# Kernel optimization log

Measured on AMD Instinct MI355X. Metric: run time of the kernel, lower is better.

Reference implementation:

```python
import jax, jax.numpy as jnp
import numpy as np

N_USERS = 100_000
N_ITEMS = 50_000
CHANNEL = 64
N_EDGES = 2_000_000
LAYERS = 3


def setup_inputs() -> dict:
    key = jax.random.key(0)
    k1, k2, k3, k4, k5 = jax.random.split(key, 5)
    user_emb = jax.random.normal(k1, (N_USERS, CHANNEL), dtype=jnp.float32) * 0.1
    item_emb = jax.random.normal(k2, (N_ITEMS, CHANNEL), dtype=jnp.float32) * 0.1
    u_idx = jax.random.randint(k3, (N_EDGES,), 0, N_USERS, dtype=jnp.int32)
    i_idx = jax.random.randint(k4, (N_EDGES,), 0, N_ITEMS, dtype=jnp.int32)
    inter_edge = jnp.stack([u_idx, i_idx], axis=0)  # [2, E]
    inter_edge_w = jax.random.uniform(k5, (N_EDGES,), dtype=jnp.float32)
    return {
        "layers_num": LAYERS,
        "user_emb": user_emb,
        "item_emb": item_emb,
        "inter_edge": inter_edge,
        "inter_edge_w": inter_edge_w,
    }


def reference(layers_num, user_emb, item_emb, inter_edge, inter_edge_w):
    """AttnHGCN.forward_ui (eval mode: no sparse dropout).

    Per layer: gather neighbor embeddings via edge index, scale by edge weight,
    scatter-sum into the other side of the bipartite graph. Residual mean over
    all layer outputs (including input embeddings).
    """
    n_users = user_emb.shape[0]
    n_items = item_emb.shape[0]
    u_idx = inter_edge[0]  # [E] user index per edge
    i_idx = inter_edge[1]  # [E] item index per edge
    w = inter_edge_w[:, None]  # [E, 1]

    u, it = user_emb, item_emb
    user_acc, item_acc = user_emb, item_emb
    for _ in range(layers_num):
        item_agg = w * it[i_idx]  # [E, C] messages item -> user
        user_agg = w * u[u_idx]   # [E, C] messages user -> item
        u = jax.ops.segment_sum(item_agg, u_idx, num_segments=n_users)
        it = jax.ops.segment_sum(user_agg, i_idx, num_segments=n_items)
        user_acc = user_acc + u
        item_acc = item_acc + it

    inv = 1.0 / (layers_num + 1)
    return item_acc * inv, user_acc * inv
```

## Files before the change

kernel.cpp:

```cpp
#include <hip/hip_runtime.h>


constexpr int N_USERS = 100000;
constexpr int N_ITEMS = 50000;
constexpr int CH      = 64;
constexpr int N_EDGES = 2000000;
constexpr int LAYERS  = 3;
constexpr int NROWS   = N_USERS + N_ITEMS;
constexpr int NDIR    = 2 * N_EDGES;

constexpr int QEDGES  = N_EDGES / 4;
constexpr int NBLK    = (QEDGES + 1023) / 1024;

constexpr int FWIN    = 512;
constexpr int FROWS   = (NROWS + FWIN - 1) / FWIN;
constexpr int NFB     = FWIN * NBLK;

constexpr int WCAP    = 9216;

constexpr long long ITEM_ELEMS = (long long)N_ITEMS * CH;
constexpr long long USER_ELEMS = (long long)N_USERS * CH;
constexpr long long TOT_ELEMS  = ITEM_ELEMS + USER_ELEMS;

typedef int      v4i __attribute__((ext_vector_type(4)));
typedef float    v4f __attribute__((ext_vector_type(4)));
typedef float    v8f __attribute__((ext_vector_type(8)));
typedef _Float16 v4h __attribute__((ext_vector_type(4)));
typedef _Float16 v8h __attribute__((ext_vector_type(8)));

static __device__ __forceinline__ float w15_to_f(unsigned pk) {
  unsigned short us = (unsigned short)(pk & 0x7FFF);
  _Float16 h;
  __builtin_memcpy(&h, &us, 2);
  return (float)h;
}
static __device__ __forceinline__ unsigned pack_sw(int src, _Float16 hw) {
  unsigned short us;
  __builtin_memcpy(&us, &hw, 2);
  return ((unsigned)src << 15) | (us & 0x7FFF);
}


__global__ __launch_bounds__(256) void scanA_kernel(
    const int* __restrict__ in, int* __restrict__ out,
    int* __restrict__ blksums, int n) {
  __shared__ int sh[256];
  int t = threadIdx.x;
  int i = blockIdx.x * 256 + t;
  int v = (i < n) ? in[i] : 0;
  int x = v;
  sh[t] = x; __syncthreads();
  for (int d = 1; d < 256; d <<= 1) {
    int add = (t >= d) ? sh[t - d] : 0;
    __syncthreads();
    x += add; sh[t] = x;
    __syncthreads();
  }
  if (i < n) out[i] = x - v;
  if (t == 255) blksums[blockIdx.x] = x;
}

__global__ __launch_bounds__(1024) void scanB_kernel(int* __restrict__ blksums, int n2) {
  __shared__ int sh[1024];
  int t = threadIdx.x;
  int v = (t < n2) ? blksums[t] : 0;
  int x = v;
  sh[t] = x; __syncthreads();
  for (int d = 1; d < 1024; d <<= 1) {
    int add = (t >= d) ? sh[t - d] : 0;
    __syncthreads();
    x += add; sh[t] = x;
    __syncthreads();
  }
  if (t < n2) blksums[t] = x - v;
}

__global__ __launch_bounds__(256) void winscanC_kernel(
    int* __restrict__ out, const int* __restrict__ blksums, int n) {
  int i = blockIdx.x * 256 + threadIdx.x;
  if (i < n) out[i] += blksums[i >> 8];
}


__global__ __launch_bounds__(1024) void bincnt1024(
    const int* __restrict__ u_idx, const int* __restrict__ i_idx,
    int* __restrict__ blkfine) {
  __shared__ int cnt[FWIN];
  const int t = threadIdx.x;
  if (t < FWIN) cnt[t] = 0;
  __syncthreads();
  int q = blockIdx.x * 1024 + t;
  if (q < QEDGES) {
    v4i u  = *(const v4i*)(u_idx + 4 * (long long)q);
    v4i it = *(const v4i*)(i_idx + 4 * (long long)q);
    atomicAdd(&cnt[u.x / FROWS], 1);
    atomicAdd(&cnt[u.y / FROWS], 1);
    atomicAdd(&cnt[u.z / FROWS], 1);
    atomicAdd(&cnt[u.w / FROWS], 1);
    atomicAdd(&cnt[(N_USERS + it.x) / FROWS], 1);
    atomicAdd(&cnt[(N_USERS + it.y) / FROWS], 1);
    atomicAdd(&cnt[(N_USERS + it.z) / FROWS], 1);
    atomicAdd(&cnt[(N_USERS + it.w) / FROWS], 1);
  }
  __syncthreads();
  if (t < FWIN) blkfine[(long long)t * NBLK + blockIdx.x] = cnt[t];
}

__global__ __launch_bounds__(256) void fineoff_ext(
    const int* __restrict__ blkfine, int* __restrict__ fineoff) {
  int i = blockIdx.x * 256 + threadIdx.x;
  if (i < FWIN) fineoff[i] = blkfine[(long long)i * NBLK];
  if (i == FWIN) fineoff[FWIN] = NDIR;
}

__global__ __launch_bounds__(1024) void segwrite1024(
    const int* __restrict__ u_idx, const int* __restrict__ i_idx,
    const float* __restrict__ wv, const int* __restrict__ blkfine,
    int* __restrict__ segkey, _Float16* __restrict__ segw) {
  extern __shared__ char smem[];
  int*            skey = (int*)smem;
  _Float16*       sw   = (_Float16*)(skey + 8192);
  unsigned short* sfin = (unsigned short*)(sw + 8192);
  int*            cnt  = (int*)(sfin + 8192);

  const int t   = threadIdx.x;
  const int blk = blockIdx.x;
  if (t < FWIN) cnt[t] = 0;
  __syncthreads();

  int q = blk * 1024 + t;
  bool valid = (q < QEDGES);
  int key8[8], fin8[8], rank8[8];
  _Float16 hw8[8];
  if (valid) {
    v4i u  = *(const v4i*)(u_idx + 4 * (long long)q);
    v4i it = *(const v4i*)(i_idx + 4 * (long long)q);
    v4f w  = *(const v4f*)(wv + 4 * (long long)q);
    int rows[8], srcs[8];
    float ws[8];
    rows[0] = u.x; rows[1] = u.y; rows[2] = u.z; rows[3] = u.w;
    srcs[0] = it.x; srcs[1] = it.y; srcs[2] = it.z; srcs[3] = it.w;
    rows[4] = N_USERS + it.x; rows[5] = N_USERS + it.y;
    rows[6] = N_USERS + it.z; rows[7] = N_USERS + it.w;
    srcs[4] = u.x; srcs[5] = u.y; srcs[6] = u.z; srcs[7] = u.w;
    ws[0] = w.x; ws[1] = w.y; ws[2] = w.z; ws[3] = w.w;
    ws[4] = w.x; ws[5] = w.y; ws[6] = w.z; ws[7] = w.w;
#pragma unroll
    for (int k = 0; k < 8; ++k) {
      int fin = rows[k] / FROWS;
      int dl  = rows[k] - fin * FROWS;
      fin8[k]  = fin;
      key8[k]  = (dl << 18) | ((k >= 4) ? (1 << 17) : 0) | srcs[k];
      hw8[k]   = (_Float16)ws[k];
      rank8[k] = atomicAdd(&cnt[fin], 1);
    }
  }
  __syncthreads();

  int v = 0, x = 0;
  if (t < FWIN) { v = cnt[t]; x = v; }
  for (int d = 1; d < FWIN; d <<= 1) {
    int add = (t < FWIN && t >= d) ? cnt[t - d] : 0;
    __syncthreads();
    if (t < FWIN) { x += add; cnt[t] = x; }
    __syncthreads();
  }
  if (t < FWIN) cnt[t] = x - v;
  __syncthreads();

  if (valid) {
#pragma unroll
    for (int k = 0; k < 8; ++k) {
      int slot = cnt[fin8[k]] + rank8[k];
      skey[slot] = key8[k];
      sw[slot]   = hw8[k];
      sfin[slot] = (unsigned short)fin8[k];
    }
  }
  __syncthreads();

  const int ecount = 8 * min(1024, QEDGES - blk * 1024);
  for (int j = t; j < ecount; j += 1024) {
    int f = sfin[j];
    int gpos = blkfine[(long long)f * NBLK + blk] + (j - cnt[f]);
    segkey[gpos] = skey[j];
    segw[gpos]   = sw[j];
  }
}

__global__ __launch_bounds__(1024) void win_sort512(
    const int* __restrict__ segkey, const _Float16* __restrict__ segw,
    const int* __restrict__ fineoff, int* __restrict__ row_ptr,
    unsigned* __restrict__ csrp) {
  __shared__ unsigned        lkey[WCAP];
  __shared__ unsigned short  lwb[WCAP];
  __shared__ int             hist[FWIN];
  const int w   = blockIdx.x;
  const int wlo = w * FROWS;
  const int wsz = min(FROWS, NROWS - wlo);
  const int s0  = fineoff[w], s1 = fineoff[w + 1];
  const int n   = s1 - s0;
  const bool inlds = (n <= WCAP);
  const int t   = threadIdx.x;

  if (t < FWIN) hist[t] = 0;
  if (inlds) {
    for (int i = t; i < n; i += 1024) {
      lkey[i] = (unsigned)segkey[s0 + i];
      _Float16 h = segw[s0 + i];
      unsigned short us;
      __builtin_memcpy(&us, &h, 2);
      lwb[i] = us;
    }
  }
  __syncthreads();

  if (inlds) {
    for (int i = t; i < n; i += 1024) atomicAdd(&hist[lkey[i] >> 18], 1);
  } else {
    for (int i = t; i < n; i += 1024)
      atomicAdd(&hist[((unsigned)segkey[s0 + i]) >> 18], 1);
  }
  __syncthreads();

  int v = 0, x = 0;
  if (t < FWIN) { v = hist[t]; x = v; }
  for (int d = 1; d < FWIN; d <<= 1) {
    int add = (t < FWIN && t >= d) ? hist[t - d] : 0;
    __syncthreads();
    if (t < FWIN) { x += add; hist[t] = x; }
    __syncthreads();
  }
  __syncthreads();
  int base = x - v;
  if (t < wsz) row_ptr[wlo + t] = s0 + base;
  if (w == FWIN - 1 && t == 0) row_ptr[NROWS] = NDIR;
  if (t < FWIN) hist[t] = s0 + base;
  __syncthreads();

  if (inlds) {
    for (int i = t; i < n; i += 1024) {
      unsigned key = lkey[i];
      int p = atomicAdd(&hist[key >> 18], 1);
      csrp[p] = ((key & 0x1FFFFu) << 15) | (lwb[i] & 0x7FFF);
    }
  } else {
    for (int i = t; i < n; i += 1024) {
      unsigned key = (unsigned)segkey[s0 + i];
      int p = atomicAdd(&hist[key >> 18], 1);
      csrp[p] = pack_sw(key & 0x1FFFF, segw[s0 + i]);
    }
  }
}

__global__ __launch_bounds__(256) void cvt_tab(
    const float* __restrict__ it, const float* __restrict__ u,
    _Float16* __restrict__ t0) {
  long long i = (long long)blockIdx.x * 256 + threadIdx.x;
  if (i >= TOT_ELEMS / 4) return;
  long long e = i * 4;
  const float* src = (e < ITEM_ELEMS) ? (it + e) : (u + (e - ITEM_ELEMS));
  v4f f = *(const v4f*)src;
  v4h h = {(_Float16)f.x, (_Float16)f.y, (_Float16)f.z, (_Float16)f.w};
  *(v4h*)(t0 + e) = h;
}

template <int MODE>
__global__ __launch_bounds__(256) void gather_fused(
    const _Float16* __restrict__ tab,
    _Float16* __restrict__ dst,
    const _Float16* __restrict__ e0,
    const _Float16* __restrict__ e1,
    float* __restrict__ out,
    const unsigned* __restrict__ csrp,
    const int* __restrict__ row_ptr) {
  int row = blockIdx.x * 4 + (threadIdx.x >> 6);
  if (row >= NROWS) return;
  int lane = threadIdx.x & 63;
  int slot = lane >> 3;
  int c8   = (lane & 7) * 8;

  const _Float16* gtab;
  long long own;
  if (row < N_USERS) {
    gtab = tab;
    own  = ITEM_ELEMS + (long long)row * CH;
  } else {
    gtab = tab + ITEM_ELEMS;
    own  = (long long)(row - N_USERS) * CH;
  }

  int beg = row_ptr[row], end = row_ptr[row + 1];
  float acc[8];
#pragma unroll
  for (int k = 0; k < 8; ++k) acc[k] = 0.f;
  int j = beg + slot;
  for (; j + 8 < end; j += 16) {
    unsigned p0 = csrp[j];
    unsigned p1 = csrp[j + 8];
    v8h h0 = *(const v8h*)(gtab + (long long)(p0 >> 15) * CH + c8);
    v8h h1 = *(const v8h*)(gtab + (long long)(p1 >> 15) * CH + c8);
    float w0 = w15_to_f(p0);
    float w1 = w15_to_f(p1);
#pragma unroll
    for (int k = 0; k < 8; ++k) acc[k] += w0 * (float)h0[k];
#pragma unroll
    for (int k = 0; k < 8; ++k) acc[k] += w1 * (float)h1[k];
  }
  if (j < end) {
    unsigned p0 = csrp[j];
    float we = w15_to_f(p0);
    v8h h = *(const v8h*)(gtab + (long long)(p0 >> 15) * CH + c8);
#pragma unroll
    for (int k = 0; k < 8; ++k) acc[k] += we * (float)h[k];
  }
#pragma unroll
  for (int off = 8; off < 64; off <<= 1) {
#pragma unroll
    for (int k = 0; k < 8; ++k) acc[k] += __shfl_xor(acc[k], off, 64);
  }
  if (slot == 0) {
    if (MODE < 2) {
      v8h hd;
#pragma unroll
      for (int k = 0; k < 8; ++k) hd[k] = (_Float16)acc[k];
      *(v8h*)(dst + own + c8) = hd;
    } else {
      const float s = 1.0f / (LAYERS + 1);
      v8h a0 = *(const v8h*)(e0 + own + c8);
      v8h a1 = *(const v8h*)(e1 + own + c8);
      v8h a2 = *(const v8h*)(tab + own + c8);
      v8f o;
#pragma unroll
      for (int k = 0; k < 8; ++k)
        o[k] = ((float)a0[k] + (float)a1[k] + (float)a2[k] + acc[k]) * s;
      *(v8f*)(out + own + c8) = o;
    }
  }
}


__global__ __launch_bounds__(256) void atomic_scatter_kernel(
    const float* __restrict__ src, float* __restrict__ dst,
    const int* __restrict__ u_idx, const int* __restrict__ i_idx,
    const float* __restrict__ w) {
  long long tid = (long long)blockIdx.x * blockDim.x + threadIdx.x;
  int edge = (int)(tid >> 4);
  if (edge >= N_EDGES) return;
  int c = ((int)tid & 15) * 4;
  int ui = u_idx[edge], ii = i_idx[edge];
  float we = w[edge];
  float4 itv = *(const float4*)(src + (long long)ii * CH + c);
  float4 uv  = *(const float4*)(src + ITEM_ELEMS + (long long)ui * CH + c);
  float* ud = dst + ITEM_ELEMS + (long long)ui * CH + c;
  float* id = dst + (long long)ii * CH + c;
  unsafeAtomicAdd(ud + 0, we * itv.x);
  unsafeAtomicAdd(ud + 1, we * itv.y);
  unsafeAtomicAdd(ud + 2, we * itv.z);
  unsafeAtomicAdd(ud + 3, we * itv.w);
  unsafeAtomicAdd(id + 0, we * uv.x);
  unsafeAtomicAdd(id + 1, we * uv.y);
  unsafeAtomicAdd(id + 2, we * uv.z);
  unsafeAtomicAdd(id + 3, we * uv.w);
}

__global__ __launch_bounds__(256) void add_scale_kernel(
    float* __restrict__ acc, const float* __restrict__ add, float s, long long n4) {
  long long i = (long long)blockIdx.x * blockDim.x + threadIdx.x;
  if (i >= n4) return;
  float4 a = ((const float4*)acc)[i];
  float4 b = ((const float4*)add)[i];
  a.x = (a.x + b.x) * s;
  a.y = (a.y + b.y) * s;
  a.z = (a.z + b.z) * s;
  a.w = (a.w + b.w) * s;
  ((float4*)acc)[i] = a;
}

extern "C" void kernel_launch(void* const* d_in, const int* in_sizes, int n_in,
                              void* d_out, int out_size, void* d_ws, size_t ws_size,
                              hipStream_t stream) {
  const float* user_emb = (const float*)d_in[1];
  const float* item_emb = (const float*)d_in[2];
  const int*   edges    = (const int*)d_in[3];
  const int*   u_idx    = edges;
  const int*   i_idx    = edges + N_EDGES;
  const float* w        = (const float*)d_in[4];

  float* out = (float*)d_out;

  float* buf_a   = (float*)d_ws;
  float* buf_b   = buf_a + TOT_ELEMS;
  float* csr_rg  = buf_b + TOT_ELEMS;
  int*   ibase   = (int*)(csr_rg + 2 * (size_t)NDIR);
  const size_t needed =
      ((size_t)2 * TOT_ELEMS + 2 * (size_t)NDIR + 3 * (size_t)NROWS + 1 + 1024) * 4;

  int*      segkey  = (int*)buf_a;
  _Float16* segw    = (_Float16*)(segkey + NDIR);
  unsigned* csrp    = (unsigned*)csr_rg;
  int*      fineoff = ibase;
  int*      row_ptr = ibase + NROWS;
  int*      blkfine = (int*)buf_b;
  int*      bsumsF  = blkfine + NFB;
  _Float16* t0 = (_Float16*)buf_a;
  _Float16* t1 = t0 + TOT_ELEMS;
  _Float16* t2 = (_Float16*)buf_b;

  if (ws_size >= needed) {
    bincnt1024<<<NBLK, 1024, 0, stream>>>(u_idx, i_idx, blkfine);
    const int nbF = (NFB + 255) / 256;
    scanA_kernel<<<nbF, 256, 0, stream>>>(blkfine, blkfine, bsumsF, NFB);
    scanB_kernel<<<1, 1024, 0, stream>>>(bsumsF, nbF);
    winscanC_kernel<<<nbF, 256, 0, stream>>>(blkfine, bsumsF, NFB);
    fineoff_ext<<<3, 256, 0, stream>>>(blkfine, fineoff);
    const size_t seg_smem = 8192 * 4 + 8192 * 2 + 8192 * 2 + FWIN * 4;
    segwrite1024<<<NBLK, 1024, seg_smem, stream>>>(
        u_idx, i_idx, w, blkfine, segkey, segw);

    win_sort512<<<FWIN, 1024, 0, stream>>>(
        segkey, segw, fineoff, row_ptr, csrp);

    const int cvt_blocks = (int)((TOT_ELEMS / 4 + 255) / 256);
    cvt_tab<<<cvt_blocks, 256, 0, stream>>>(item_emb, user_emb, t0);

    const int gather_blocks = (NROWS + 3) / 4;
    gather_fused<0><<<gather_blocks, 256, 0, stream>>>(
        t0, t1, nullptr, nullptr, nullptr, csrp, row_ptr);
    gather_fused<1><<<gather_blocks, 256, 0, stream>>>(
        t1, t2, nullptr, nullptr, nullptr, csrp, row_ptr);
    gather_fused<2><<<gather_blocks, 256, 0, stream>>>(
        t2, nullptr, t0, t1, out, csrp, row_ptr);
  } else {
    const size_t item_bytes = (size_t)ITEM_ELEMS * sizeof(float);
    const size_t user_bytes = (size_t)USER_ELEMS * sizeof(float);
    hipMemcpyAsync(buf_a,              item_emb, item_bytes, hipMemcpyDeviceToDevice, stream);
    hipMemcpyAsync(buf_a + ITEM_ELEMS, user_emb, user_bytes, hipMemcpyDeviceToDevice, stream);
    hipMemcpyAsync(out,                item_emb, item_bytes, hipMemcpyDeviceToDevice, stream);
    hipMemcpyAsync(out + ITEM_ELEMS,   user_emb, user_bytes, hipMemcpyDeviceToDevice, stream);
    const long long st = (long long)N_EDGES * 16;
    const int sb = (int)((st + 255) / 256);
    const long long n4 = TOT_ELEMS / 4;
    const int add_blocks = (int)((n4 + 255) / 256);
    float* src = buf_a;
    float* dst = buf_b;
    for (int l = 0; l < LAYERS; ++l) {
      hipMemsetAsync(dst, 0, (size_t)TOT_ELEMS * sizeof(float), stream);
      atomic_scatter_kernel<<<sb, 256, 0, stream>>>(src, dst, u_idx, i_idx, w);
      const float s = (l == LAYERS - 1) ? (1.0f / (LAYERS + 1)) : 1.0f;
      add_scale_kernel<<<add_blocks, 256, 0, stream>>>(out, dst, s, n4);
      float* t = src; src = dst; dst = t;
    }
  }
}
```

Measured before the change: 378.0 us.

## Double row-window count to 1024 and drop fineoff extraction kernel

Raises the number of row windows used by the CSR-building bucket sort from 512 to 1024, so each window holds fewer edges and the per-window sort has twice as many blocks to spread across the GPU. The scans and counting kernels are widened to 1024-entry histograms, and the key packing drops the direction bit to free room for a narrower local row field. The separate fineoff extraction kernel is removed; window bounds are read directly from the scanned block counts. The risk is a larger block-count array to scan and a smaller LDS capacity per window, so more windows may fall back to the slower global-memory path.

```diff
diff --git a/kernel.cpp b/kernel.cpp
--- a/kernel.cpp
+++ b/kernel.cpp
@@ -12,11 +12,11 @@
 constexpr int QEDGES  = N_EDGES / 4;
 constexpr int NBLK    = (QEDGES + 1023) / 1024;
 
-constexpr int FWIN    = 512;
+constexpr int FWIN    = 1024;
 constexpr int FROWS   = (NROWS + FWIN - 1) / FWIN;
 constexpr int NFB     = FWIN * NBLK;
 
-constexpr int WCAP    = 9216;
+constexpr int WCAP    = 8192;
 
 constexpr long long ITEM_ELEMS = (long long)N_ITEMS * CH;
 constexpr long long USER_ELEMS = (long long)N_USERS * CH;
@@ -41,23 +41,23 @@
 }
 
 
-__global__ __launch_bounds__(256) void scanA_kernel(
+__global__ __launch_bounds__(512) void scanA512(
     const int* __restrict__ in, int* __restrict__ out,
     int* __restrict__ blksums, int n) {
-  __shared__ int sh[256];
+  __shared__ int sh[512];
   int t = threadIdx.x;
-  int i = blockIdx.x * 256 + t;
+  int i = blockIdx.x * 512 + t;
   int v = (i < n) ? in[i] : 0;
   int x = v;
   sh[t] = x; __syncthreads();
-  for (int d = 1; d < 256; d <<= 1) {
+  for (int d = 1; d < 512; d <<= 1) {
     int add = (t >= d) ? sh[t - d] : 0;
     __syncthreads();
     x += add; sh[t] = x;
     __syncthreads();
   }
   if (i < n) out[i] = x - v;
-  if (t == 255) blksums[blockIdx.x] = x;
+  if (t == 511) blksums[blockIdx.x] = x;
 }
 
 __global__ __launch_bounds__(1024) void scanB_kernel(int* __restrict__ blksums, int n2) {
@@ -75,10 +75,10 @@
   if (t < n2) blksums[t] = x - v;
 }
 
-__global__ __launch_bounds__(256) void winscanC_kernel(
+__global__ __launch_bounds__(512) void winscanC512(
     int* __restrict__ out, const int* __restrict__ blksums, int n) {
-  int i = blockIdx.x * 256 + threadIdx.x;
-  if (i < n) out[i] += blksums[i >> 8];
+  int i = blockIdx.x * 512 + threadIdx.x;
+  if (i < n) out[i] += blksums[i >> 9];
 }
 
 
@@ -87,7 +87,7 @@
     int* __restrict__ blkfine) {
   __shared__ int cnt[FWIN];
   const int t = threadIdx.x;
-  if (t < FWIN) cnt[t] = 0;
+  cnt[t] = 0;
   __syncthreads();
   int q = blockIdx.x * 1024 + t;
   if (q < QEDGES) {
@@ -103,14 +103,7 @@
     atomicAdd(&cnt[(N_USERS + it.w) / FROWS], 1);
   }
   __syncthreads();
-  if (t < FWIN) blkfine[(long long)t * NBLK + blockIdx.x] = cnt[t];
-}
-
-__global__ __launch_bounds__(256) void fineoff_ext(
-    const int* __restrict__ blkfine, int* __restrict__ fineoff) {
-  int i = blockIdx.x * 256 + threadIdx.x;
-  if (i < FWIN) fineoff[i] = blkfine[(long long)i * NBLK];
-  if (i == FWIN) fineoff[FWIN] = NDIR;
+  blkfine[(long long)t * NBLK + blockIdx.x] = cnt[t];
 }
 
 __global__ __launch_bounds__(1024) void segwrite1024(
@@ -125,7 +118,7 @@
 
   const int t   = threadIdx.x;
   const int blk = blockIdx.x;
-  if (t < FWIN) cnt[t] = 0;
+  cnt[t] = 0;
   __syncthreads();
 
   int q = blk * 1024 + t;
@@ -150,22 +143,21 @@
       int fin = rows[k] / FROWS;
       int dl  = rows[k] - fin * FROWS;
       fin8[k]  = fin;
-      key8[k]  = (dl << 18) | ((k >= 4) ? (1 << 17) : 0) | srcs[k];
+      key8[k]  = (dl << 17) | srcs[k];
       hw8[k]   = (_Float16)ws[k];
       rank8[k] = atomicAdd(&cnt[fin], 1);
     }
   }
   __syncthreads();
 
-  int v = 0, x = 0;
-  if (t < FWIN) { v = cnt[t]; x = v; }
-  for (int d = 1; d < FWIN; d <<= 1) {
-    int add = (t < FWIN && t >= d) ? cnt[t - d] : 0;
-    __syncthreads();
-    if (t < FWIN) { x += add; cnt[t] = x; }
-    __syncthreads();
-  }
-  if (t < FWIN) cnt[t] = x - v;
+  int v = cnt[t], x = v;
+  for (int d = 1; d < 1024; d <<= 1) {
+    int add = (t >= d) ? cnt[t - d] : 0;
+    __syncthreads();
+    x += add; cnt[t] = x;
+    __syncthreads();
+  }
+  cnt[t] = x - v;
   __syncthreads();
 
   if (valid) {
@@ -188,9 +180,9 @@
   }
 }
 
-__global__ __launch_bounds__(1024) void win_sort512(
+__global__ __launch_bounds__(1024) void win_sort1024(
     const int* __restrict__ segkey, const _Float16* __restrict__ segw,
-    const int* __restrict__ fineoff, int* __restrict__ row_ptr,
+    const int* __restrict__ blkfine, int* __restrict__ row_ptr,
     unsigned* __restrict__ csrp) {
   __shared__ unsigned        lkey[WCAP];
   __shared__ unsigned short  lwb[WCAP];
@@ -198,12 +190,13 @@
   const int w   = blockIdx.x;
   const int wlo = w * FROWS;
   const int wsz = min(FROWS, NROWS - wlo);
-  const int s0  = fineoff[w], s1 = fineoff[w + 1];
+  const int s0  = blkfine[(long long)w * NBLK];
+  const int s1  = (w < FWIN - 1) ? blkfine[(long long)(w + 1) * NBLK] : NDIR;
   const int n   = s1 - s0;
   const bool inlds = (n <= WCAP);
   const int t   = threadIdx.x;
 
-  if (t < FWIN) hist[t] = 0;
+  hist[t] = 0;
   if (inlds) {
     for (int i = t; i < n; i += 1024) {
       lkey[i] = (unsigned)segkey[s0 + i];
@@ -216,38 +209,37 @@
   __syncthreads();
 
   if (inlds) {
-    for (int i = t; i < n; i += 1024) atomicAdd(&hist[lkey[i] >> 18], 1);
+    for (int i = t; i < n; i += 1024) atomicAdd(&hist[lkey[i] >> 17], 1);
   } else {
     for (int i = t; i < n; i += 1024)
-      atomicAdd(&hist[((unsigned)segkey[s0 + i]) >> 18], 1);
-  }
-  __syncthreads();
-
-  int v = 0, x = 0;
-  if (t < FWIN) { v = hist[t]; x = v; }
-  for (int d = 1; d < FWIN; d <<= 1) {
-    int add = (t < FWIN && t >= d) ? hist[t - d] : 0;
-    __syncthreads();
-    if (t < FWIN) { x += add; hist[t] = x; }
+      atomicAdd(&hist[((unsigned)segkey[s0 + i]) >> 17], 1);
+  }
+  __syncthreads();
+
+  int v = hist[t], x = v;
+  for (int d = 1; d < 1024; d <<= 1) {
+    int add = (t >= d) ? hist[t - d] : 0;
+    __syncthreads();
+    x += add; hist[t] = x;
     __syncthreads();
   }
   __syncthreads();
   int base = x - v;
   if (t < wsz) row_ptr[wlo + t] = s0 + base;
   if (w == FWIN - 1 && t == 0) row_ptr[NROWS] = NDIR;
-  if (t < FWIN) hist[t] = s0 + base;
+  hist[t] = s0 + base;
   __syncthreads();
 
   if (inlds) {
     for (int i = t; i < n; i += 1024) {
       unsigned key = lkey[i];
-      int p = atomicAdd(&hist[key >> 18], 1);
+      int p = atomicAdd(&hist[key >> 17], 1);
       csrp[p] = ((key & 0x1FFFFu) << 15) | (lwb[i] & 0x7FFF);
     }
   } else {
     for (int i = t; i < n; i += 1024) {
       unsigned key = (unsigned)segkey[s0 + i];
-      int p = atomicAdd(&hist[key >> 18], 1);
+      int p = atomicAdd(&hist[key >> 17], 1);
       csrp[p] = pack_sw(key & 0x1FFFF, segw[s0 + i]);
     }
   }
@@ -399,8 +391,7 @@
   int*      segkey  = (int*)buf_a;
   _Float16* segw    = (_Float16*)(segkey + NDIR);
   unsigned* csrp    = (unsigned*)csr_rg;
-  int*      fineoff = ibase;
-  int*      row_ptr = ibase + NROWS;
+  int*      row_ptr = ibase;
   int*      blkfine = (int*)buf_b;
   int*      bsumsF  = blkfine + NFB;
   _Float16* t0 = (_Float16*)buf_a;
@@ -409,17 +400,16 @@
 
   if (ws_size >= needed) {
     bincnt1024<<<NBLK, 1024, 0, stream>>>(u_idx, i_idx, blkfine);
-    const int nbF = (NFB + 255) / 256;
-    scanA_kernel<<<nbF, 256, 0, stream>>>(blkfine, blkfine, bsumsF, NFB);
+    const int nbF = (NFB + 511) / 512;
+    scanA512<<<nbF, 512, 0, stream>>>(blkfine, blkfine, bsumsF, NFB);
     scanB_kernel<<<1, 1024, 0, stream>>>(bsumsF, nbF);
-    winscanC_kernel<<<nbF, 256, 0, stream>>>(blkfine, bsumsF, NFB);
-    fineoff_ext<<<3, 256, 0, stream>>>(blkfine, fineoff);
+    winscanC512<<<nbF, 512, 0, stream>>>(blkfine, bsumsF, NFB);
     const size_t seg_smem = 8192 * 4 + 8192 * 2 + 8192 * 2 + FWIN * 4;
     segwrite1024<<<NBLK, 1024, seg_smem, stream>>>(
         u_idx, i_idx, w, blkfine, segkey, segw);
 
-    win_sort512<<<FWIN, 1024, 0, stream>>>(
-        segkey, segw, fineoff, row_ptr, csrp);
+    win_sort1024<<<FWIN, 1024, 0, stream>>>(
+        segkey, segw, blkfine, row_ptr, csrp);
 
     const int cvt_blocks = (int)((TOT_ELEMS / 4 + 255) / 256);
     cvt_tab<<<cvt_blocks, 256, 0, stream>>>(item_emb, user_emb, t0);
```

Measured after the change: 386.0 us. 1.02x slower.
